# Kernel tuning notes

Measured on AMD Instinct MI355X. Metric: run time of the kernel, lower is better.

## Reference

```python
import jax, jax.numpy as jnp
import numpy as np

B, NMAX, H, C, HID = 256, 512, 256, 64, 512
NEG = jnp.float32(-1e9)

def setup_inputs() -> dict:
    key = jax.random.key(0)
    ks = jax.random.split(key, 12)
    s_in = 1.0 / np.sqrt(2 * H + C)
    s_h = 1.0 / np.sqrt(HID)
    return {
        "nodes_hv": jax.random.normal(ks[0], (B, NMAX, H), jnp.float32),
        "class_cond": jax.random.normal(ks[1], (B, C), jnp.float32),
        "W1": jax.random.normal(ks[2], (2 * H + C, HID), jnp.float32) * s_in,
        "b1": jnp.zeros((HID,), jnp.float32),
        "W2": jax.random.normal(ks[3], (HID, HID), jnp.float32) * s_h,
        "b2": jnp.zeros((HID,), jnp.float32),
        "W3": jax.random.normal(ks[4], (HID, 1), jnp.float32) * s_h,
        "b3": jnp.zeros((1,), jnp.float32),
        "dirns": jax.random.randint(ks[5], (B,), 0, 2, jnp.int32),
        "node_counts": jax.random.randint(ks[6], (B,), NMAX // 2 + 1, NMAX, jnp.int32),
        "dests": jax.random.randint(ks[7], (B,), 0, NMAX // 2, jnp.int32),
    }

def reference(nodes_hv, class_cond, W1, b1, W2, b2, W3, b3, dirns, node_counts, dests):
    Bb, Nmax, Hh = nodes_hv.shape
    D = Nmax - 1  # padded number of candidate destinations
    # per-graph newest node embedding: hv[b, n_b - 1]
    src_idx = (node_counts - 1).astype(jnp.int32)
    src_embed = jnp.take_along_axis(nodes_hv, src_idx[:, None, None], axis=1)  # [B,1,H]
    src_b = jnp.broadcast_to(src_embed, (Bb, D, Hh))
    cand = nodes_hv[:, :D, :]  # candidate (old-node) embeddings, padded
    # dirn == 1: edge new->old, so (src_side, dest_side) = (cand, new); else (new, cand)
    dirn1 = (dirns == 1)[:, None, None]
    side_a = jnp.where(dirn1, cand, src_b)
    side_b = jnp.where(dirn1, src_b, cand)
    cc = jnp.broadcast_to(class_cond[:, None, :], (Bb, D, class_cond.shape[-1]))
    x = jnp.concatenate([side_a, side_b, cc], axis=2)  # [B, D, 2H+C]
    h = jax.nn.relu(jnp.einsum("bdi,ih->bdh", x, W1) + b1)
    h = jax.nn.relu(jnp.einsum("bdi,ih->bdh", h, W2) + b2)
    scores = (jnp.einsum("bdi,io->bdo", h, W3) + b3)[..., 0]  # [B, D]
    # ragged validity: graph b has n_b - 1 candidates
    valid = jnp.arange(D)[None, :] < (node_counts - 1)[:, None]
    scores = jnp.where(valid, scores, NEG)
    logp = jax.nn.log_softmax(scores, axis=1)
    loss = -jnp.take_along_axis(logp, dests[:, None].astype(jnp.int32), axis=1)[:, 0]  # [B]
    return loss
```

## Files before the change

kernel.cpp:

```cpp
#include <hip/hip_runtime.h>
#include <math.h>

#define BB    256
#define NMAX  512
#define HH    256
#define CC    64
#define HID   512
#define NEGV  -1000000000.0f
#define MT    64
#define NW    8
#define SA_LD 264
#define TILE  512
#define KSTR  (32 * TILE)

typedef __attribute__((ext_vector_type(8))) short short8;
typedef __attribute__((ext_vector_type(4))) float floatx4;

__device__ inline ushort f2bf(float x) {
    unsigned u = __float_as_uint(x);
    u = (u + 0x7FFFu + ((u >> 16) & 1u)) >> 16;
    return (ushort)u;
}

__global__ __launch_bounds__(256) void prep_kernel(
    const float* __restrict__ W1, const float* __restrict__ W2,
    ushort* __restrict__ Wt1s, ushort* __restrict__ Wt2s,
    const float* __restrict__ nodes_hv, const float* __restrict__ class_cond,
    const float* __restrict__ b1,
    const int* __restrict__ dirns, const int* __restrict__ node_counts,
    float* __restrict__ v_ws)
{
    const int blk = blockIdx.x;
    const int t = threadIdx.x;

    __shared__ float s_conv[32][68];
    __shared__ float s_src[HH];
    __shared__ float s_cc[CC];

    if (blk < 256) {
        const float* W = (blk < 128) ? W1 : W2;
        ushort* out    = (blk < 128) ? Wt1s : Wt2s;
        const int bb  = blk & 127;
        const int kb  = bb >> 3, ntg = bb & 7;

        {
            const int kl = t >> 3, nn = (t & 7) * 8;
            const float* src = W + (size_t)(kb * 32 + kl) * HID + ntg * 64 + nn;
            *(float4*)&s_conv[kl][nn]     = *(const float4*)src;
            *(float4*)&s_conv[kl][nn + 4] = *(const float4*)(src + 4);
        }
        __syncthreads();

        const int ntl = t >> 6, ls = t & 63;
        const int qs = ls >> 4, l15s = ls & 15;
        short8 o;
        #pragma unroll
        for (int j = 0; j < 8; ++j)
            o[j] = (short)f2bf(s_conv[qs * 8 + j][ntl * 16 + l15s]);
        const int nt = ntg * 4 + ntl;
        *(short8*)(out + ((size_t)(kb * 32 + nt)) * TILE + ls * 8) = o;
    } else {
        const int b = blk - 256;
        const int nc   = node_counts[b];
        const int dirn = dirns[b];
        const int src_idx = nc - 1;

        s_src[t] = nodes_hv[((size_t)b * NMAX + src_idx) * HH + t];
        if (t < CC) s_cc[t] = class_cond[b * CC + t];
        __syncthreads();

        const int srcoff = (dirn == 1) ? HH : 0;

        const int j = 2 * t;
        float acc0 = b1[j];
        float acc1 = b1[j + 1];

        #pragma unroll 4
        for (int r = 0; r < HH; ++r) {
            const float s = s_src[r];
            const float* wp = W1 + (size_t)(srcoff + r) * HID + j;
            acc0 += s * wp[0];
            acc1 += s * wp[1];
        }
        #pragma unroll 4
        for (int c = 0; c < CC; ++c) {
            const float s = s_cc[c];
            const float* wp = W1 + (size_t)(2 * HH + c) * HID + j;
            acc0 += s * wp[0];
            acc1 += s * wp[1];
        }
        v_ws[b * HID + j]     = acc0;
        v_ws[b * HID + j + 1] = acc1;
    }
}

__global__ __launch_bounds__(512, 4) void mlp2(
    const float* __restrict__ nodes_hv,
    const ushort* __restrict__ Wt1s, const ushort* __restrict__ Wt2s,
    const float* __restrict__ b2, const float* __restrict__ W3,
    const float* __restrict__ b3,
    const int* __restrict__ dirns, const int* __restrict__ node_counts,
    const float* __restrict__ v_ws, float* __restrict__ scores)
{
    const int b  = blockIdx.y;
    const int d0 = blockIdx.x * MT;
    const int t  = threadIdx.x;
    const int lane = t & 63, wv = t >> 6;
    const int l15 = lane & 15, q = lane >> 4;

    __shared__ ushort s_u[32768];

    const int nc = node_counts[b];

    if (d0 >= nc - 1) {
        if (t < MT) scores[b * NMAX + d0 + t] = NEGV;
        return;
    }

    const int kb0 = (dirns[b] == 1) ? 0 : 8;

    {
        const float4* src4 = (const float4*)nodes_hv + ((size_t)b * NMAX + d0) * (HH / 4);
        #pragma unroll
        for (int i = 0; i < (MT * HH / 4) / 512; ++i) {
            int idx = t + i * 512;
            int row = idx >> 6, c4 = idx & 63;
            float4 v = src4[idx];
            ushort4 p;
            p.x = f2bf(v.x); p.y = f2bf(v.y); p.z = f2bf(v.z); p.w = f2bf(v.w);
            *(ushort4*)&s_u[row * SA_LD + c4 * 4] = p;
        }
    }
    __syncthreads();

    floatx4 acc[4][4];
    #pragma unroll
    for (int mb = 0; mb < 4; ++mb)
        #pragma unroll
        for (int tn = 0; tn < 4; ++tn)
            acc[mb][tn] = (floatx4){0.f, 0.f, 0.f, 0.f};

    {
        const ushort* wb1 = Wt1s + ((size_t)kb0 * 32 + wv * 4) * TILE + lane * 8;
        #pragma unroll
        for (int ks = 0; ks < 8; ++ks) {
            const ushort* wp = wb1 + (size_t)ks * KSTR;
            short8 bfr[4];
            #pragma unroll
            for (int tn = 0; tn < 4; ++tn)
                bfr[tn] = *(const short8*)(wp + tn * TILE);
            short8 a[4];
            #pragma unroll
            for (int mb = 0; mb < 4; ++mb)
                a[mb] = *(const short8*)&s_u[(mb * 16 + l15) * SA_LD + ks * 32 + q * 8];
            #pragma unroll
            for (int tn = 0; tn < 4; ++tn)
                #pragma unroll
                for (int mb = 0; mb < 4; ++mb)
                    acc[mb][tn] = __builtin_amdgcn_mfma_f32_16x16x32_bf16(a[mb], bfr[tn], acc[mb][tn], 0, 0, 0);
        }
    }
    __syncthreads();

    const int n0 = wv * 64;

    {
        const int j_w = l15 & 7;
        #pragma unroll
        for (int tn = 0; tn < 4; ++tn) {
            const int n = n0 + tn * 16 + l15;
            const float v = v_ws[b * HID + n];
            const int ks_w = wv * 2 + (tn >> 1);
            const int qr   = ((tn & 1) << 1) + (l15 >> 3);
            #pragma unroll
            for (int mb = 0; mb < 4; ++mb) {
                #pragma unroll
                for (int r = 0; r < 4; ++r) {
                    float h = acc[mb][tn][r] + v;
                    h = h > 0.f ? h : 0.f;
                    s_u[((mb * 16 + ks_w) * 64 + qr * 16 + q * 4 + r) * 8 + j_w] = f2bf(h);
                }
            }
        }
    }
    __syncthreads();

    #pragma unroll
    for (int mb = 0; mb < 4; ++mb)
        #pragma unroll
        for (int tn = 0; tn < 4; ++tn)
            acc[mb][tn] = (floatx4){0.f, 0.f, 0.f, 0.f};
    {
        const ushort* wb2 = Wt2s + ((size_t)wv * 4) * TILE + lane * 8;
        #pragma unroll
        for (int ks = 0; ks < 16; ++ks) {
            const ushort* wp = wb2 + (size_t)ks * KSTR;
            short8 bfr[4];
            #pragma unroll
            for (int tn = 0; tn < 4; ++tn)
                bfr[tn] = *(const short8*)(wp + tn * TILE);
            short8 a[4];
            #pragma unroll
            for (int mb = 0; mb < 4; ++mb)
                a[mb] = *(const short8*)&s_u[((mb * 16 + ks) * 64 + lane) * 8];
            #pragma unroll
            for (int tn = 0; tn < 4; ++tn)
                #pragma unroll
                for (int mb = 0; mb < 4; ++mb)
                    acc[mb][tn] = __builtin_amdgcn_mfma_f32_16x16x32_bf16(a[mb], bfr[tn], acc[mb][tn], 0, 0, 0);
        }
    }

    float p[4][4] = {{0,0,0,0},{0,0,0,0},{0,0,0,0},{0,0,0,0}};
    #pragma unroll
    for (int tn = 0; tn < 4; ++tn) {
        const int n  = n0 + tn * 16 + l15;
        const float bb = b2[n];
        const float w3 = W3[n];
        #pragma unroll
        for (int mb = 0; mb < 4; ++mb)
            #pragma unroll
            for (int r = 0; r < 4; ++r) {
                float h = acc[mb][tn][r] + bb;
                h = h > 0.f ? h : 0.f;
                p[mb][r] += h * w3;
            }
    }
    __syncthreads();
    float* s_red = (float*)s_u;
    #pragma unroll
    for (int mb = 0; mb < 4; ++mb)
        #pragma unroll
        for (int r = 0; r < 4; ++r) {
            float v = p[mb][r];
            v += __shfl_xor(v, 1, 64);
            v += __shfl_xor(v, 2, 64);
            v += __shfl_xor(v, 4, 64);
            v += __shfl_xor(v, 8, 64);
            if (l15 == 0) s_red[wv * MT + mb * 16 + q * 4 + r] = v;
        }
    __syncthreads();
    if (t < MT) {
        float s = b3[0];
        #pragma unroll
        for (int w = 0; w < NW; ++w) s += s_red[w * MT + t];
        const int d = d0 + t;
        scores[b * NMAX + d] = (d < nc - 1) ? s : NEGV;
    }
}

__global__ __launch_bounds__(256) void loss_kernel(
    const float* __restrict__ scores, const int* __restrict__ dests,
    float* __restrict__ out)
{
    const int b = blockIdx.x;
    const int t = threadIdx.x;
    __shared__ float red[4];

    const float s0 = scores[b * NMAX + t];
    const float s1 = scores[b * NMAX + t + 256];

    const int lane = t & 63, wv = t >> 6;

    float mx = fmaxf(s0, s1);
    #pragma unroll
    for (int off = 32; off > 0; off >>= 1) mx = fmaxf(mx, __shfl_down(mx, off, 64));
    if (lane == 0) red[wv] = mx;
    __syncthreads();
    mx = fmaxf(fmaxf(red[0], red[1]), fmaxf(red[2], red[3]));
    __syncthreads();

    float e = __expf(s0 - mx) + __expf(s1 - mx);
    #pragma unroll
    for (int off = 32; off > 0; off >>= 1) e += __shfl_down(e, off, 64);
    if (lane == 0) red[wv] = e;
    __syncthreads();

    if (t == 0) {
        const float sum = red[0] + red[1] + red[2] + red[3];
        const float sd = scores[b * NMAX + dests[b]];
        out[b] = -(sd - mx - logf(sum));
    }
}

extern "C" void kernel_launch(void* const* d_in, const int* in_sizes, int n_in,
                              void* d_out, int out_size, void* d_ws, size_t ws_size,
                              hipStream_t stream) {
    const float* nodes_hv    = (const float*)d_in[0];
    const float* class_cond  = (const float*)d_in[1];
    const float* W1          = (const float*)d_in[2];
    const float* b1          = (const float*)d_in[3];
    const float* W2          = (const float*)d_in[4];
    const float* b2          = (const float*)d_in[5];
    const float* W3          = (const float*)d_in[6];
    const float* b3          = (const float*)d_in[7];
    const int*   dirns       = (const int*)d_in[8];
    const int*   node_counts = (const int*)d_in[9];
    const int*   dests       = (const int*)d_in[10];
    float* out = (float*)d_out;

    ushort* Wt1s   = (ushort*)d_ws;
    ushort* Wt2s   = Wt1s + 16 * KSTR;
    float*  v_ws   = (float*)(Wt2s + 16 * KSTR);
    float*  scores = v_ws + BB * HID;

    prep_kernel<<<512, 256, 0, stream>>>(W1, W2, Wt1s, Wt2s,
                                         nodes_hv, class_cond, b1,
                                         dirns, node_counts, v_ws);
    mlp2<<<dim3(NMAX / MT, BB), 512, 0, stream>>>(
        nodes_hv, Wt1s, Wt2s, b2, W3, b3, dirns, node_counts, v_ws, scores);
    loss_kernel<<<BB, 256, 0, stream>>>(scores, dests, out);
}
```

Before: 318.2 us.

## Switch MLP GEMMs from 16x16x32 to 32x32x16 bf16 MFMA tiles

Replaces the 16x16x32 MFMA tiling (4x4 accumulators per wave) with 32x32x16 MFMA instructions (2x2 accumulators of 16 floats). The weight pre-swizzle in the prep kernel, the LDS layout for the layer-1 output, the epilogue row mapping and the reduction shuffles are all rewritten to match the new fragment layout. The A-tile LDS pitch also changes. The aim is fewer MFMA issues and fewer LDS/global fragment loads per unit of work. The risk is LDS bank conflicts, since the new pitch of 258 gives 16-byte reads that are not 16-byte aligned.

```diff
diff --git a/kernel.cpp b/kernel.cpp
--- a/kernel.cpp
+++ b/kernel.cpp
@@ -9,12 +9,12 @@
 #define NEGV  -1000000000.0f
 #define MT    64
 #define NW    8
-#define SA_LD 264
+#define SA_LD 258
 #define TILE  512
-#define KSTR  (32 * TILE)
-
-typedef __attribute__((ext_vector_type(8))) short short8;
-typedef __attribute__((ext_vector_type(4))) float floatx4;
+#define KSTR  (16 * TILE)
+
+typedef __attribute__((ext_vector_type(8)))  short  short8;
+typedef __attribute__((ext_vector_type(16))) float  floatx16;
 
 __device__ inline ushort f2bf(float x) {
     unsigned u = __float_as_uint(x);
@@ -51,14 +51,15 @@
         }
         __syncthreads();
 
-        const int ntl = t >> 6, ls = t & 63;
-        const int qs = ls >> 4, l15s = ls & 15;
+        const int tile_l = t >> 6, ls = t & 63;
+        const int kh_l = tile_l >> 1, nt_l = tile_l & 1;
+        const int q5s = ls >> 5, l31s = ls & 31;
         short8 o;
         #pragma unroll
         for (int j = 0; j < 8; ++j)
-            o[j] = (short)f2bf(s_conv[qs * 8 + j][ntl * 16 + l15s]);
-        const int nt = ntg * 4 + ntl;
-        *(short8*)(out + ((size_t)(kb * 32 + nt)) * TILE + ls * 8) = o;
+            o[j] = (short)f2bf(s_conv[kh_l * 16 + q5s * 8 + j][nt_l * 32 + l31s]);
+        const int kh = kb * 2 + kh_l, nt = ntg * 2 + nt_l;
+        *(short8*)(out + ((size_t)kh * 16 + nt) * TILE + ls * 8) = o;
     } else {
         const int b = blk - 256;
         const int nc   = node_counts[b];
@@ -106,7 +107,7 @@
     const int d0 = blockIdx.x * MT;
     const int t  = threadIdx.x;
     const int lane = t & 63, wv = t >> 6;
-    const int l15 = lane & 15, q = lane >> 4;
+    const int l31 = lane & 31, q5 = lane >> 5;
 
     __shared__ ushort s_u[32768];
 
@@ -117,7 +118,7 @@
         return;
     }
 
-    const int kb0 = (dirns[b] == 1) ? 0 : 8;
+    const int kh0 = (dirns[b] == 1) ? 0 : 16;
 
     {
         const float4* src4 = (const float4*)nodes_hv + ((size_t)b * NMAX + d0) * (HH / 4);
@@ -133,52 +134,48 @@
     }
     __syncthreads();
 
-    floatx4 acc[4][4];
-    #pragma unroll
-    for (int mb = 0; mb < 4; ++mb)
-        #pragma unroll
-        for (int tn = 0; tn < 4; ++tn)
-            acc[mb][tn] = (floatx4){0.f, 0.f, 0.f, 0.f};
+    floatx16 acc[2][2];
+    #pragma unroll
+    for (int mt = 0; mt < 2; ++mt)
+        #pragma unroll
+        for (int nt = 0; nt < 2; ++nt)
+            #pragma unroll
+            for (int r = 0; r < 16; ++r)
+                acc[mt][nt][r] = 0.f;
 
     {
-        const ushort* wb1 = Wt1s + ((size_t)kb0 * 32 + wv * 4) * TILE + lane * 8;
-        #pragma unroll
-        for (int ks = 0; ks < 8; ++ks) {
-            const ushort* wp = wb1 + (size_t)ks * KSTR;
-            short8 bfr[4];
+        const ushort* wb1 = Wt1s + ((size_t)kh0 * 16 + wv * 2) * TILE + lane * 8;
+        #pragma unroll
+        for (int kh = 0; kh < 16; ++kh) {
+            const ushort* wp = wb1 + (size_t)kh * KSTR;
+            short8 b0 = *(const short8*)(wp);
+            short8 b1f = *(const short8*)(wp + TILE);
+            short8 a0 = *(const short8*)&s_u[(l31)      * SA_LD + kh * 16 + q5 * 8];
+            short8 a1 = *(const short8*)&s_u[(32 + l31) * SA_LD + kh * 16 + q5 * 8];
+            acc[0][0] = __builtin_amdgcn_mfma_f32_32x32x16_bf16(a0, b0,  acc[0][0], 0, 0, 0);
+            acc[0][1] = __builtin_amdgcn_mfma_f32_32x32x16_bf16(a0, b1f, acc[0][1], 0, 0, 0);
+            acc[1][0] = __builtin_amdgcn_mfma_f32_32x32x16_bf16(a1, b0,  acc[1][0], 0, 0, 0);
+            acc[1][1] = __builtin_amdgcn_mfma_f32_32x32x16_bf16(a1, b1f, acc[1][1], 0, 0, 0);
+        }
+    }
+    __syncthreads();
+
+    {
+        #pragma unroll
+        for (int nt = 0; nt < 2; ++nt) {
+            const int n = wv * 64 + nt * 32 + l31;
+            const float v = v_ws[b * HID + n];
+            const int kh2 = n >> 4;
+            const int q2p = (n >> 3) & 1;
+            const int j_w = n & 7;
             #pragma unroll
-            for (int tn = 0; tn < 4; ++tn)
-                bfr[tn] = *(const short8*)(wp + tn * TILE);
-            short8 a[4];
-            #pragma unroll
-            for (int mb = 0; mb < 4; ++mb)
-                a[mb] = *(const short8*)&s_u[(mb * 16 + l15) * SA_LD + ks * 32 + q * 8];
-            #pragma unroll
-            for (int tn = 0; tn < 4; ++tn)
+            for (int mt = 0; mt < 2; ++mt) {
                 #pragma unroll
-                for (int mb = 0; mb < 4; ++mb)
-                    acc[mb][tn] = __builtin_amdgcn_mfma_f32_16x16x32_bf16(a[mb], bfr[tn], acc[mb][tn], 0, 0, 0);
-        }
-    }
-    __syncthreads();
-
-    const int n0 = wv * 64;
-
-    {
-        const int j_w = l15 & 7;
-        #pragma unroll
-        for (int tn = 0; tn < 4; ++tn) {
-            const int n = n0 + tn * 16 + l15;
-            const float v = v_ws[b * HID + n];
-            const int ks_w = wv * 2 + (tn >> 1);
-            const int qr   = ((tn & 1) << 1) + (l15 >> 3);
-            #pragma unroll
-            for (int mb = 0; mb < 4; ++mb) {
-                #pragma unroll
-                for (int r = 0; r < 4; ++r) {
-                    float h = acc[mb][tn][r] + v;
+                for (int reg = 0; reg < 16; ++reg) {
+                    const int l31w = (reg & 3) + 8 * (reg >> 2) + 4 * q5;
+                    float h = acc[mt][nt][reg] + v;
                     h = h > 0.f ? h : 0.f;
-                    s_u[((mb * 16 + ks_w) * 64 + qr * 16 + q * 4 + r) * 8 + j_w] = f2bf(h);
+                    s_u[((kh2 * 2 + mt) * 64 + q2p * 32 + l31w) * 8 + j_w] = f2bf(h);
                 }
             }
         }
@@ -186,58 +183,64 @@
     __syncthreads();
 
     #pragma unroll
-    for (int mb = 0; mb < 4; ++mb)
-        #pragma unroll
-        for (int tn = 0; tn < 4; ++tn)
-            acc[mb][tn] = (floatx4){0.f, 0.f, 0.f, 0.f};
+    for (int mt = 0; mt < 2; ++mt)
+        #pragma unroll
+        for (int nt = 0; nt < 2; ++nt)
+            #pragma unroll
+            for (int r = 0; r < 16; ++r)
+                acc[mt][nt][r] = 0.f;
     {
-        const ushort* wb2 = Wt2s + ((size_t)wv * 4) * TILE + lane * 8;
-        #pragma unroll
-        for (int ks = 0; ks < 16; ++ks) {
-            const ushort* wp = wb2 + (size_t)ks * KSTR;
-            short8 bfr[4];
-            #pragma unroll
-            for (int tn = 0; tn < 4; ++tn)
-                bfr[tn] = *(const short8*)(wp + tn * TILE);
-            short8 a[4];
-            #pragma unroll
-            for (int mb = 0; mb < 4; ++mb)
-                a[mb] = *(const short8*)&s_u[((mb * 16 + ks) * 64 + lane) * 8];
-            #pragma unroll
-            for (int tn = 0; tn < 4; ++tn)
-                #pragma unroll
-                for (int mb = 0; mb < 4; ++mb)
-                    acc[mb][tn] = __builtin_amdgcn_mfma_f32_16x16x32_bf16(a[mb], bfr[tn], acc[mb][tn], 0, 0, 0);
-        }
-    }
-
-    float p[4][4] = {{0,0,0,0},{0,0,0,0},{0,0,0,0},{0,0,0,0}};
-    #pragma unroll
-    for (int tn = 0; tn < 4; ++tn) {
-        const int n  = n0 + tn * 16 + l15;
+        const ushort* wb2 = Wt2s + ((size_t)wv * 2) * TILE + lane * 8;
+        #pragma unroll
+        for (int kh2 = 0; kh2 < 32; ++kh2) {
+            const ushort* wp = wb2 + (size_t)kh2 * KSTR;
+            short8 b0 = *(const short8*)(wp);
+            short8 b1f = *(const short8*)(wp + TILE);
+            short8 a0 = *(const short8*)&s_u[((kh2 * 2 + 0) * 64 + lane) * 8];
+            short8 a1 = *(const short8*)&s_u[((kh2 * 2 + 1) * 64 + lane) * 8];
+            acc[0][0] = __builtin_amdgcn_mfma_f32_32x32x16_bf16(a0, b0,  acc[0][0], 0, 0, 0);
+            acc[0][1] = __builtin_amdgcn_mfma_f32_32x32x16_bf16(a0, b1f, acc[0][1], 0, 0, 0);
+            acc[1][0] = __builtin_amdgcn_mfma_f32_32x32x16_bf16(a1, b0,  acc[1][0], 0, 0, 0);
+            acc[1][1] = __builtin_amdgcn_mfma_f32_32x32x16_bf16(a1, b1f, acc[1][1], 0, 0, 0);
+        }
+    }
+
+    float p[2][16];
+    #pragma unroll
+    for (int mt = 0; mt < 2; ++mt)
+        #pragma unroll
+        for (int r = 0; r < 16; ++r)
+            p[mt][r] = 0.f;
+    #pragma unroll
+    for (int nt = 0; nt < 2; ++nt) {
+        const int n  = wv * 64 + nt * 32 + l31;
         const float bb = b2[n];
         const float w3 = W3[n];
         #pragma unroll
-        for (int mb = 0; mb < 4; ++mb)
+        for (int mt = 0; mt < 2; ++mt)
             #pragma unroll
-            for (int r = 0; r < 4; ++r) {
-                float h = acc[mb][tn][r] + bb;
+            for (int r = 0; r < 16; ++r) {
+                float h = acc[mt][nt][r] + bb;
                 h = h > 0.f ? h : 0.f;
-                p[mb][r] += h * w3;
+                p[mt][r] += h * w3;
             }
     }
     __syncthreads();
     float* s_red = (float*)s_u;
     #pragma unroll
-    for (int mb = 0; mb < 4; ++mb)
-        #pragma unroll
-        for (int r = 0; r < 4; ++r) {
-            float v = p[mb][r];
+    for (int mt = 0; mt < 2; ++mt)
+        #pragma unroll
+        for (int r = 0; r < 16; ++r) {
+            float v = p[mt][r];
             v += __shfl_xor(v, 1, 64);
             v += __shfl_xor(v, 2, 64);
             v += __shfl_xor(v, 4, 64);
             v += __shfl_xor(v, 8, 64);
-            if (l15 == 0) s_red[wv * MT + mb * 16 + q * 4 + r] = v;
+            v += __shfl_xor(v, 16, 64);
+            if (l31 == 0) {
+                const int row = mt * 32 + (r & 3) + 8 * (r >> 2) + 4 * q5;
+                s_red[wv * MT + row] = v;
+            }
         }
     __syncthreads();
     if (t < MT) {
@@ -300,8 +303,8 @@
     float* out = (float*)d_out;
 
     ushort* Wt1s   = (ushort*)d_ws;
-    ushort* Wt2s   = Wt1s + 16 * KSTR;
-    float*  v_ws   = (float*)(Wt2s + 16 * KSTR);
+    ushort* Wt2s   = Wt1s + 32 * KSTR;
+    float*  v_ws   = (float*)(Wt2s + 32 * KSTR);
     float*  scores = v_ws + BB * HID;
 
     prep_kernel<<<512, 256, 0, stream>>>(W1, W2, Wt1s, Wt2s,
```

Result: slower. 337.0 us (+5.9%).
